# Optimization experiments

Measured on AMD Instinct MI355X. Metric: run time of the kernel, lower is better.

Reference implementation:

```python
import jax, jax.numpy as jnp
import numpy as np

B, S, D = 2, 2048, 1024
H = 16
HD = D // H  # 64

def setup_inputs() -> dict:
    key = jax.random.key(0)
    ks = jax.random.split(key, 6)
    s = 1.0 / np.sqrt(D)
    return {
        "x": jax.random.normal(ks[0], (B, S, D), dtype=jnp.float32),
        "Wq": jax.random.normal(ks[1], (D, D), dtype=jnp.float32) * s,
        "Wk": jax.random.normal(ks[2], (D, D), dtype=jnp.float32) * s,
        "Wv": jax.random.normal(ks[3], (D, D), dtype=jnp.float32) * s,
        "Wo": jax.random.normal(ks[4], (D, D), dtype=jnp.float32) * s,
        "bo": jax.random.normal(ks[5], (D,), dtype=jnp.float32) * 0.01,
    }

def reference(x, Wq, Wk, Wv, Wo, bo):
    b, n, _ = x.shape
    # qkv projections (nn.Linear: x @ W^T, no bias for qkv)
    q = (x @ Wq.T).reshape(b, n, H, HD).transpose(0, 2, 1, 3)  # [B,H,S,hd]
    k = (x @ Wk.T).reshape(b, n, H, HD).transpose(0, 2, 1, 3)
    v = (x @ Wv.T).reshape(b, n, H, HD).transpose(0, 2, 1, 3)
    scores = jnp.einsum('bhqd,bhkd->bhqk', q, k)  # [B,H,S,S]
    causal = jnp.triu(jnp.ones((n, n), dtype=bool), k=1)
    scores = jnp.where(causal, -jnp.inf, scores)
    attn = jax.nn.softmax(scores / np.sqrt(HD), axis=-1)
    ctx = jnp.einsum('bhqk,bhkd->bhqd', attn, v)  # [B,H,S,hd]
    ctx = ctx.transpose(0, 2, 1, 3).reshape(b, n, D)
    return ctx @ Wo.T + bo
```

## Files before the change

kernel.cpp:

```cpp
#include <hip/hip_runtime.h>
#include <hip/hip_bf16.h>

typedef __hip_bfloat16 bf16;
typedef short v8s __attribute__((ext_vector_type(8)));
typedef float v4f __attribute__((ext_vector_type(4)));

#define S_ 2048
#define D_ 1024
#define H_ 16
#define HD_ 64

#define EXP2F(x) __builtin_amdgcn_exp2f(x)
#define NEG_BIG (-1.0e30f)
#define C2 0.1803368801111244f

#define GLDS16(g, l) __builtin_amdgcn_global_load_lds(                        \
    (const __attribute__((address_space(1))) unsigned int*)(g),               \
    (__attribute__((address_space(3))) unsigned int*)(l), 16, 0, 0)

static __device__ __forceinline__ unsigned short bf16_bits(bf16 h) {
    union { bf16 h; unsigned short u; } c; c.h = h; return c.u;
}

static __device__ __forceinline__ v8s pack_bf16x8(const float4 a, const float4 b) {
    union { v8s v; unsigned short u[8]; } r;
    r.u[0] = bf16_bits(__float2bfloat16(a.x));
    r.u[1] = bf16_bits(__float2bfloat16(a.y));
    r.u[2] = bf16_bits(__float2bfloat16(a.z));
    r.u[3] = bf16_bits(__float2bfloat16(a.w));
    r.u[4] = bf16_bits(__float2bfloat16(b.x));
    r.u[5] = bf16_bits(__float2bfloat16(b.y));
    r.u[6] = bf16_bits(__float2bfloat16(b.z));
    r.u[7] = bf16_bits(__float2bfloat16(b.w));
    return r.v;
}

__global__ __launch_bounds__(256)
void cvt_bf16(const float* __restrict__ x,  const float* __restrict__ wq,
              const float* __restrict__ wk, const float* __restrict__ wv,
              const float* __restrict__ wo,
              bf16* __restrict__ xb,  bf16* __restrict__ wqb,
              bf16* __restrict__ wkb, bf16* __restrict__ wvb,
              bf16* __restrict__ wob)
{
    const int seg = blockIdx.y;
    const float* src; bf16* dst; int n;
    switch (seg) {
        case 0: src = x;  dst = xb;  n = 4096 * 1024; break;
        case 1: src = wq; dst = wqb; n = 1024 * 1024; break;
        case 2: src = wk; dst = wkb; n = 1024 * 1024; break;
        case 3: src = wv; dst = wvb; n = 1024 * 1024; break;
        default:src = wo; dst = wob; n = 1024 * 1024; break;
    }
    const int idx = (blockIdx.x * 256 + threadIdx.x) * 8;
    if (idx >= n) return;
    *(v8s*)&dst[idx] = pack_bf16x8(*(const float4*)&src[idx],
                                   *(const float4*)&src[idx + 4]);
}

__global__ __launch_bounds__(256)
void gemm_qkv_f(const bf16* __restrict__ xb, const bf16* __restrict__ wqb,
                const bf16* __restrict__ wkb, const bf16* __restrict__ wvb,
                bf16* __restrict__ qd, bf16* __restrict__ kd, bf16* __restrict__ vtd)
{
    const int mode = blockIdx.z;
    const bf16* __restrict__ W = (mode == 0) ? wqb : (mode == 1) ? wkb : wvb;
    const int m0 = blockIdx.x * 128;
    const int n0 = blockIdx.y * 128;
    __shared__ bf16 As[128 * 32];
    __shared__ bf16 Bs[128 * 32];
    const int t    = threadIdx.x;
    const int lane = t & 63, w = t >> 6;
    const int wr = w >> 1, wc = w & 1;
    const int l15 = lane & 15, quad = lane >> 4;
    const int r16 = lane >> 2, c8 = (lane & 3) * 8;
    v4f acc[4][4] = {};

    const bf16* ga = &xb[(m0 + w*16 + r16) * 1024 + c8];
    const bf16* gb = &W [(n0 + w*16 + r16) * 1024 + c8];
    bf16* la0 = &As[w * 16 * 32];
    bf16* la1 = &As[(64 + w * 16) * 32];
    bf16* lb0 = &Bs[w * 16 * 32];
    bf16* lb1 = &Bs[(64 + w * 16) * 32];

    for (int k0 = 0; k0 < 1024; k0 += 32) {
        __syncthreads();
        GLDS16(ga + k0,             la0);
        GLDS16(ga + k0 + 64 * 1024, la1);
        GLDS16(gb + k0,             lb0);
        GLDS16(gb + k0 + 64 * 1024, lb1);
        __syncthreads();
        v8s a[4], b[4];
#pragma unroll
        for (int mt = 0; mt < 4; mt++) a[mt] = *(const v8s*)&As[(wr*64 + mt*16 + l15)*32 + quad*8];
#pragma unroll
        for (int nt = 0; nt < 4; nt++) b[nt] = *(const v8s*)&Bs[(wc*64 + nt*16 + l15)*32 + quad*8];
#pragma unroll
        for (int mt = 0; mt < 4; mt++)
#pragma unroll
            for (int nt = 0; nt < 4; nt++)
                acc[mt][nt] = __builtin_amdgcn_mfma_f32_16x16x32_bf16(a[mt], b[nt], acc[mt][nt], 0, 0, 0);
    }

    const float qscale = (mode == 0) ? C2 : 1.0f;
#pragma unroll
    for (int mt = 0; mt < 4; mt++) {
        const int mb = m0 + wr*64 + mt*16 + quad*4;
        const int b_ = mb >> 11, s = mb & 2047;
#pragma unroll
        for (int nt = 0; nt < 4; nt++) {
            const int n = n0 + wc*64 + nt*16 + l15;
            const int h = n >> 6, d = n & 63;
            if (mode == 2) {
                unsigned int lo = (unsigned int)bf16_bits(__float2bfloat16(acc[mt][nt][0]))
                                | ((unsigned int)bf16_bits(__float2bfloat16(acc[mt][nt][1])) << 16);
                unsigned int hi = (unsigned int)bf16_bits(__float2bfloat16(acc[mt][nt][2]))
                                | ((unsigned int)bf16_bits(__float2bfloat16(acc[mt][nt][3])) << 16);
                uint2 pv; pv.x = lo; pv.y = hi;
                *(uint2*)&vtd[((b_*H_ + h)*HD_ + d)*S_ + s] = pv;
            } else {
                bf16* __restrict__ dst = (mode == 0) ? qd : kd;
#pragma unroll
                for (int r = 0; r < 4; r++)
                    dst[((b_*H_ + h)*S_ + (s + r))*HD_ + d] = __float2bfloat16(acc[mt][nt][r] * qscale);
            }
        }
    }
}

__global__ __launch_bounds__(256)
void gemm_out_f(const bf16* __restrict__ ctx, const bf16* __restrict__ wob,
                const float* __restrict__ bo, float* __restrict__ out)
{
    const int m0 = blockIdx.x * 128;
    const int n0 = blockIdx.y * 128;
    __shared__ bf16 As[128 * 32];
    __shared__ bf16 Bs[128 * 32];
    const int t    = threadIdx.x;
    const int lane = t & 63, w = t >> 6;
    const int wr = w >> 1, wc = w & 1;
    const int l15 = lane & 15, quad = lane >> 4;
    const int r16 = lane >> 2, c8 = (lane & 3) * 8;
    v4f acc[4][4] = {};

    const bf16* ga = &ctx[(m0 + w*16 + r16) * 1024 + c8];
    const bf16* gb = &wob[(n0 + w*16 + r16) * 1024 + c8];
    bf16* la0 = &As[w * 16 * 32];
    bf16* la1 = &As[(64 + w * 16) * 32];
    bf16* lb0 = &Bs[w * 16 * 32];
    bf16* lb1 = &Bs[(64 + w * 16) * 32];

    for (int k0 = 0; k0 < 1024; k0 += 32) {
        __syncthreads();
        GLDS16(ga + k0,             la0);
        GLDS16(ga + k0 + 64 * 1024, la1);
        GLDS16(gb + k0,             lb0);
        GLDS16(gb + k0 + 64 * 1024, lb1);
        __syncthreads();
        v8s a[4], b[4];
#pragma unroll
        for (int mt = 0; mt < 4; mt++) a[mt] = *(const v8s*)&As[(wr*64 + mt*16 + l15)*32 + quad*8];
#pragma unroll
        for (int nt = 0; nt < 4; nt++) b[nt] = *(const v8s*)&Bs[(wc*64 + nt*16 + l15)*32 + quad*8];
#pragma unroll
        for (int mt = 0; mt < 4; mt++)
#pragma unroll
            for (int nt = 0; nt < 4; nt++)
                acc[mt][nt] = __builtin_amdgcn_mfma_f32_16x16x32_bf16(a[mt], b[nt], acc[mt][nt], 0, 0, 0);
    }

#pragma unroll
    for (int mt = 0; mt < 4; mt++) {
        const int mb = m0 + wr*64 + mt*16 + quad*4;
#pragma unroll
        for (int nt = 0; nt < 4; nt++) {
            const int n = n0 + wc*64 + nt*16 + l15;
            const float bias = bo[n];
#pragma unroll
            for (int r = 0; r < 4; r++)
                out[(mb + r)*1024 + n] = acc[mt][nt][r] + bias;
        }
    }
}

__global__ __launch_bounds__(256)
void gemm_qkv(const float* __restrict__ x, const float* __restrict__ Wq,
              const float* __restrict__ Wk, const float* __restrict__ Wv,
              bf16* __restrict__ qd, bf16* __restrict__ kd, bf16* __restrict__ vtd)
{
    const int mode = blockIdx.z;
    const float* __restrict__ W = (mode == 0) ? Wq : (mode == 1) ? Wk : Wv;
    const int m0 = blockIdx.x * 128;
    const int n0 = blockIdx.y * 128;
    __shared__ bf16 As[128 * 40];
    __shared__ bf16 Bs[128 * 40];
    const int t    = threadIdx.x;
    const int lane = t & 63, w = t >> 6;
    const int wr = w >> 1, wc = w & 1;
    const int l15 = lane & 15, quad = lane >> 4;
    const int srow = t >> 2, scol = (t & 3) * 8;
    v4f acc[4][4] = {};

    for (int k0 = 0; k0 < 1024; k0 += 32) {
        __syncthreads();
        {
            const float* pa = &x[(m0 + srow) * 1024 + k0 + scol];
            *(v8s*)&As[srow*40 + scol] = pack_bf16x8(*(const float4*)pa, *(const float4*)(pa + 4));
            const float* pa2 = pa + 64 * 1024;
            *(v8s*)&As[(srow+64)*40 + scol] = pack_bf16x8(*(const float4*)pa2, *(const float4*)(pa2 + 4));
            const float* pb = &W[(n0 + srow) * 1024 + k0 + scol];
            *(v8s*)&Bs[srow*40 + scol] = pack_bf16x8(*(const float4*)pb, *(const float4*)(pb + 4));
            const float* pb2 = pb + 64 * 1024;
            *(v8s*)&Bs[(srow+64)*40 + scol] = pack_bf16x8(*(const float4*)pb2, *(const float4*)(pb2 + 4));
        }
        __syncthreads();
        v8s a[4], b[4];
#pragma unroll
        for (int mt = 0; mt < 4; mt++) a[mt] = *(const v8s*)&As[(wr*64 + mt*16 + l15)*40 + quad*8];
#pragma unroll
        for (int nt = 0; nt < 4; nt++) b[nt] = *(const v8s*)&Bs[(wc*64 + nt*16 + l15)*40 + quad*8];
#pragma unroll
        for (int mt = 0; mt < 4; mt++)
#pragma unroll
            for (int nt = 0; nt < 4; nt++)
                acc[mt][nt] = __builtin_amdgcn_mfma_f32_16x16x32_bf16(a[mt], b[nt], acc[mt][nt], 0, 0, 0);
    }

    const float qscale = (mode == 0) ? C2 : 1.0f;
#pragma unroll
    for (int mt = 0; mt < 4; mt++) {
        const int mb = m0 + wr*64 + mt*16 + quad*4;
        const int b_ = mb >> 11, s = mb & 2047;
#pragma unroll
        for (int nt = 0; nt < 4; nt++) {
            const int n = n0 + wc*64 + nt*16 + l15;
            const int h = n >> 6, d = n & 63;
            if (mode == 2) {
                unsigned int lo = (unsigned int)bf16_bits(__float2bfloat16(acc[mt][nt][0]))
                                | ((unsigned int)bf16_bits(__float2bfloat16(acc[mt][nt][1])) << 16);
                unsigned int hi = (unsigned int)bf16_bits(__float2bfloat16(acc[mt][nt][2]))
                                | ((unsigned int)bf16_bits(__float2bfloat16(acc[mt][nt][3])) << 16);
                uint2 pv; pv.x = lo; pv.y = hi;
                *(uint2*)&vtd[((b_*H_ + h)*HD_ + d)*S_ + s] = pv;
            } else {
                bf16* __restrict__ dst = (mode == 0) ? qd : kd;
#pragma unroll
                for (int r = 0; r < 4; r++)
                    dst[((b_*H_ + h)*S_ + (s + r))*HD_ + d] = __float2bfloat16(acc[mt][nt][r] * qscale);
            }
        }
    }
}

__global__ __launch_bounds__(256)
void gemm_out(const bf16* __restrict__ ctx, const float* __restrict__ Wo,
              const float* __restrict__ bo, float* __restrict__ out)
{
    const int m0 = blockIdx.x * 128;
    const int n0 = blockIdx.y * 128;
    __shared__ bf16 As[128 * 40];
    __shared__ bf16 Bs[128 * 40];
    const int t    = threadIdx.x;
    const int lane = t & 63, w = t >> 6;
    const int wr = w >> 1, wc = w & 1;
    const int l15 = lane & 15, quad = lane >> 4;
    const int srow = t >> 2, scol = (t & 3) * 8;
    v4f acc[4][4] = {};

    for (int k0 = 0; k0 < 1024; k0 += 32) {
        __syncthreads();
        {
            *(v8s*)&As[srow*40 + scol]      = *(const v8s*)&ctx[(m0+srow)*1024 + k0 + scol];
            *(v8s*)&As[(srow+64)*40 + scol] = *(const v8s*)&ctx[(m0+srow+64)*1024 + k0 + scol];
            const float* pb = &Wo[(n0 + srow) * 1024 + k0 + scol];
            *(v8s*)&Bs[srow*40 + scol] = pack_bf16x8(*(const float4*)pb, *(const float4*)(pb + 4));
            const float* pb2 = pb + 64 * 1024;
            *(v8s*)&Bs[(srow+64)*40 + scol] = pack_bf16x8(*(const float4*)pb2, *(const float4*)(pb2 + 4));
        }
        __syncthreads();
        v8s a[4], b[4];
#pragma unroll
        for (int mt = 0; mt < 4; mt++) a[mt] = *(const v8s*)&As[(wr*64 + mt*16 + l15)*40 + quad*8];
#pragma unroll
        for (int nt = 0; nt < 4; nt++) b[nt] = *(const v8s*)&Bs[(wc*64 + nt*16 + l15)*40 + quad*8];
#pragma unroll
        for (int mt = 0; mt < 4; mt++)
#pragma unroll
            for (int nt = 0; nt < 4; nt++)
                acc[mt][nt] = __builtin_amdgcn_mfma_f32_16x16x32_bf16(a[mt], b[nt], acc[mt][nt], 0, 0, 0);
    }

#pragma unroll
    for (int mt = 0; mt < 4; mt++) {
        const int mb = m0 + wr*64 + mt*16 + quad*4;
#pragma unroll
        for (int nt = 0; nt < 4; nt++) {
            const int n = n0 + wc*64 + nt*16 + l15;
            const float bias = bo[n];
#pragma unroll
            for (int r = 0; r < 4; r++)
                out[(mb + r)*1024 + n] = acc[mt][nt][r] + bias;
        }
    }
}

__global__ __launch_bounds__(256)
void flash_attn(const bf16* __restrict__ qd, const bf16* __restrict__ kd,
                const bf16* __restrict__ vtd, bf16* __restrict__ ctx)
{
    const int qb = 15 - blockIdx.x;
    const int bh = blockIdx.y;
    const int t = threadIdx.x;
    const int lane = t & 63, w = t >> 6;
    const int l15 = lane & 15, quad = lane >> 4;
    const int q0 = qb * 128;

    __shared__ bf16 Ks[2][64 * 72];
    __shared__ bf16 Vs[2][64 * 72];
    __shared__ bf16 Pl[4][16 * 72];

    const int mrow0 = q0 + w * 16;
    const int mrow1 = q0 + 64 + w * 16;

    v8s qf[2][2];
#pragma unroll
    for (int mt = 0; mt < 2; mt++) {
        const bf16* qb_ = qd + (bh*S_ + (mt ? mrow1 : mrow0) + l15) * HD_;
        qf[mt][0] = *(const v8s*)(qb_ + quad*8);
        qf[mt][1] = *(const v8s*)(qb_ + 32 + quad*8);
    }

    v4f o[2][4] = {};
    float ps[2][4] = {};

    const int rowlo = t >> 3, col8 = (t & 7) * 8;
    const int nT = qb * 2 + 2;

    v8s pk0 = *(const v8s*)&kd[(bh*S_ + rowlo)*HD_ + col8];
    v8s pk1 = *(const v8s*)&kd[(bh*S_ + rowlo + 32)*HD_ + col8];
    v8s pv0 = *(const v8s*)&vtd[(bh*HD_ + rowlo)*S_ + col8];
    v8s pv1 = *(const v8s*)&vtd[(bh*HD_ + rowlo + 32)*S_ + col8];

    for (int it = 0; it < nT; ++it) {
        const int c0 = it * 64;
        bf16* Kb = &Ks[it & 1][0];
        bf16* Vb = &Vs[it & 1][0];
        *(v8s*)&Kb[rowlo*72 + col8]      = pk0;
        *(v8s*)&Kb[(rowlo+32)*72 + col8] = pk1;
        *(v8s*)&Vb[rowlo*72 + col8]      = pv0;
        *(v8s*)&Vb[(rowlo+32)*72 + col8] = pv1;
        const int cn = (it + 1 < nT) ? c0 + 64 : 0;
        pk0 = *(const v8s*)&kd[(bh*S_ + cn + rowlo)*HD_ + col8];
        pk1 = *(const v8s*)&kd[(bh*S_ + cn + rowlo + 32)*HD_ + col8];
        pv0 = *(const v8s*)&vtd[(bh*HD_ + rowlo)*S_ + cn + col8];
        pv1 = *(const v8s*)&vtd[(bh*HD_ + rowlo + 32)*S_ + cn + col8];
        __syncthreads();

        if (c0 <= mrow1 + 15) {
            v8s kf[4][2];
#pragma unroll
            for (int kt = 0; kt < 4; kt++) {
                kf[kt][0] = *(const v8s*)&Kb[(kt*16 + l15)*72 + quad*8];
                kf[kt][1] = *(const v8s*)&Kb[(kt*16 + l15)*72 + 32 + quad*8];
            }
            v8s vf[4][2];
#pragma unroll
            for (int dt = 0; dt < 4; dt++) {
                vf[dt][0] = *(const v8s*)&Vs[it & 1][(dt*16 + l15)*72 + quad*8];
                vf[dt][1] = *(const v8s*)&Vs[it & 1][(dt*16 + l15)*72 + 32 + quad*8];
            }

#pragma unroll
            for (int mt = 0; mt < 2; mt++) {
                const int mr = mt ? mrow1 : mrow0;
                if (c0 > mr + 15) continue;
                v4f sc[4] = {};
#pragma unroll
                for (int kt = 0; kt < 4; kt++) {
                    sc[kt] = __builtin_amdgcn_mfma_f32_16x16x32_bf16(qf[mt][0], kf[kt][0], sc[kt], 0, 0, 0);
                    sc[kt] = __builtin_amdgcn_mfma_f32_16x16x32_bf16(qf[mt][1], kf[kt][1], sc[kt], 0, 0, 0);
                }
                const bool full = (c0 + 63 <= mr);
#pragma unroll
                for (int r = 0; r < 4; r++) {
                    const int qg = mr + quad*4 + r;
#pragma unroll
                    for (int kt = 0; kt < 4; kt++) {
                        float s = sc[kt][r];
                        if (!full) {
                            const int kg = c0 + kt*16 + l15;
                            s = (kg <= qg) ? s : NEG_BIG;
                        }
                        const float p = EXP2F(s);
                        sc[kt][r] = p;
                        ps[mt][r] += p;
                    }
                }
                bf16* pw = &Pl[w][0];
#pragma unroll
                for (int kt = 0; kt < 4; kt++)
#pragma unroll
                    for (int r = 0; r < 4; r++)
                        pw[(quad*4 + r)*72 + kt*16 + l15] = __float2bfloat16(sc[kt][r]);
                v8s pf0 = *(const v8s*)&pw[l15*72 + quad*8];
                v8s pf1 = *(const v8s*)&pw[l15*72 + 32 + quad*8];
#pragma unroll
                for (int dt = 0; dt < 4; dt++) {
                    o[mt][dt] = __builtin_amdgcn_mfma_f32_16x16x32_bf16(pf0, vf[dt][0], o[mt][dt], 0, 0, 0);
                    o[mt][dt] = __builtin_amdgcn_mfma_f32_16x16x32_bf16(pf1, vf[dt][1], o[mt][dt], 0, 0, 0);
                }
            }
        }
    }

    const int b_ = bh >> 4, h = bh & 15;
#pragma unroll
    for (int mt = 0; mt < 2; mt++) {
        const int mr = mt ? mrow1 : mrow0;
#pragma unroll
        for (int r = 0; r < 4; r++) {
            float l = ps[mt][r];
#pragma unroll
            for (int off = 1; off < 16; off <<= 1) l += __shfl_xor(l, off);
            const float linv = 1.0f / l;
            const int qg = mr + quad*4 + r;
#pragma unroll
            for (int dt = 0; dt < 4; dt++)
                ctx[(b_*S_ + qg)*D_ + h*HD_ + dt*16 + l15] = __float2bfloat16(o[mt][dt][r] * linv);
        }
    }
}

extern "C" void kernel_launch(void* const* d_in, const int* in_sizes, int n_in,
                              void* d_out, int out_size, void* d_ws, size_t ws_size,
                              hipStream_t stream) {
    const float* x  = (const float*)d_in[0];
    const float* Wq = (const float*)d_in[1];
    const float* Wk = (const float*)d_in[2];
    const float* Wv = (const float*)d_in[3];
    const float* Wo = (const float*)d_in[4];
    const float* bo = (const float*)d_in[5];
    float* out = (float*)d_out;

    const size_t SEG = (size_t)2 * H_ * S_ * HD_;
    bf16* qd  = (bf16*)d_ws;
    bf16* kd  = qd  + SEG;
    bf16* vtd = kd  + SEG;
    bf16* xc  = vtd + SEG;

    const size_t need_fast = (SEG * 4 + 4 * 1024 * 1024) * sizeof(bf16);

    if (ws_size >= need_fast) {
        bf16* wqb = xc + SEG;
        bf16* wkb = wqb + 1024 * 1024;
        bf16* wvb = wkb + 1024 * 1024;
        bf16* wob = wvb + 1024 * 1024;
        cvt_bf16<<<dim3(2048, 5), 256, 0, stream>>>(x, Wq, Wk, Wv, Wo,
                                                    xc, wqb, wkb, wvb, wob);
        gemm_qkv_f<<<dim3(32, 8, 3), 256, 0, stream>>>(xc, wqb, wkb, wvb, qd, kd, vtd);
        flash_attn<<<dim3(16, 32), 256, 0, stream>>>(qd, kd, vtd, xc);
        gemm_out_f<<<dim3(32, 8), 256, 0, stream>>>(xc, wob, bo, out);
    } else {
        gemm_qkv<<<dim3(32, 8, 3), 256, 0, stream>>>(x, Wq, Wk, Wv, qd, kd, vtd);
        flash_attn<<<dim3(16, 32), 256, 0, stream>>>(qd, kd, vtd, xc);
        gemm_out<<<dim3(32, 8), 256, 0, stream>>>(xc, Wo, bo, out);
    }
}
```

Baseline: 223.1 us.

## Split causal attention KV range across two blocks and combine partials

Each query block's KV tiles are split into two equal halves. Each half runs in its own block along grid z, which doubles the number of blocks and evens out the causal work per block. Each half writes unnormalized bf16 partial outputs and per-row exp sums to workspace. A new combine kernel adds the two halves and normalizes. This costs extra global traffic, an extra launch, a larger workspace requirement, and some precision lost by storing partials in bf16.

```diff
diff --git a/kernel.cpp b/kernel.cpp
--- a/kernel.cpp
+++ b/kernel.cpp
@@ -20,6 +20,9 @@
 
 static __device__ __forceinline__ unsigned short bf16_bits(bf16 h) {
     union { bf16 h; unsigned short u; } c; c.h = h; return c.u;
+}
+static __device__ __forceinline__ float bits2f(unsigned short u) {
+    union { float f; unsigned int i; } c; c.i = ((unsigned int)u) << 16; return c.f;
 }
 
 static __device__ __forceinline__ v8s pack_bf16x8(const float4 a, const float4 b) {
@@ -306,15 +309,21 @@
 
 __global__ __launch_bounds__(256)
 void flash_attn(const bf16* __restrict__ qd, const bf16* __restrict__ kd,
-                const bf16* __restrict__ vtd, bf16* __restrict__ ctx)
+                const bf16* __restrict__ vtd, bf16* __restrict__ outp,
+                float* __restrict__ lsum)
 {
     const int qb = 15 - blockIdx.x;
     const int bh = blockIdx.y;
+    const int split = blockIdx.z;
+    const bool dosplit = (gridDim.z == 2);
     const int t = threadIdx.x;
     const int lane = t & 63, w = t >> 6;
     const int l15 = lane & 15, quad = lane >> 4;
     const int q0 = qb * 128;
 
+    const int tbeg = dosplit ? split * (qb + 1) : 0;
+    const int tend = dosplit ? tbeg + qb + 1 : 2 * qb + 2;
+
     __shared__ bf16 Ks[2][64 * 72];
     __shared__ bf16 Vs[2][64 * 72];
     __shared__ bf16 Pl[4][16 * 72];
@@ -334,22 +343,22 @@
     float ps[2][4] = {};
 
     const int rowlo = t >> 3, col8 = (t & 7) * 8;
-    const int nT = qb * 2 + 2;
-
-    v8s pk0 = *(const v8s*)&kd[(bh*S_ + rowlo)*HD_ + col8];
-    v8s pk1 = *(const v8s*)&kd[(bh*S_ + rowlo + 32)*HD_ + col8];
-    v8s pv0 = *(const v8s*)&vtd[(bh*HD_ + rowlo)*S_ + col8];
-    v8s pv1 = *(const v8s*)&vtd[(bh*HD_ + rowlo + 32)*S_ + col8];
-
-    for (int it = 0; it < nT; ++it) {
-        const int c0 = it * 64;
+
+    int c0 = tbeg * 64;
+    v8s pk0 = *(const v8s*)&kd[(bh*S_ + c0 + rowlo)*HD_ + col8];
+    v8s pk1 = *(const v8s*)&kd[(bh*S_ + c0 + rowlo + 32)*HD_ + col8];
+    v8s pv0 = *(const v8s*)&vtd[(bh*HD_ + rowlo)*S_ + c0 + col8];
+    v8s pv1 = *(const v8s*)&vtd[(bh*HD_ + rowlo + 32)*S_ + c0 + col8];
+
+    for (int it = tbeg; it < tend; ++it) {
+        c0 = it * 64;
         bf16* Kb = &Ks[it & 1][0];
         bf16* Vb = &Vs[it & 1][0];
         *(v8s*)&Kb[rowlo*72 + col8]      = pk0;
         *(v8s*)&Kb[(rowlo+32)*72 + col8] = pk1;
         *(v8s*)&Vb[rowlo*72 + col8]      = pv0;
         *(v8s*)&Vb[(rowlo+32)*72 + col8] = pv1;
-        const int cn = (it + 1 < nT) ? c0 + 64 : 0;
+        const int cn = (it + 1 < tend) ? c0 + 64 : tbeg * 64;
         pk0 = *(const v8s*)&kd[(bh*S_ + cn + rowlo)*HD_ + col8];
         pk1 = *(const v8s*)&kd[(bh*S_ + cn + rowlo + 32)*HD_ + col8];
         pv0 = *(const v8s*)&vtd[(bh*HD_ + rowlo)*S_ + cn + col8];
@@ -414,6 +423,8 @@
     }
 
     const int b_ = bh >> 4, h = bh & 15;
+    bf16* __restrict__ po = outp + (size_t)split * (4 * 1024 * 1024);
+    float* __restrict__ ls = lsum + split * (32 * S_);
 #pragma unroll
     for (int mt = 0; mt < 2; mt++) {
         const int mr = mt ? mrow1 : mrow0;
@@ -422,13 +433,39 @@
             float l = ps[mt][r];
 #pragma unroll
             for (int off = 1; off < 16; off <<= 1) l += __shfl_xor(l, off);
-            const float linv = 1.0f / l;
             const int qg = mr + quad*4 + r;
-#pragma unroll
-            for (int dt = 0; dt < 4; dt++)
-                ctx[(b_*S_ + qg)*D_ + h*HD_ + dt*16 + l15] = __float2bfloat16(o[mt][dt][r] * linv);
-        }
-    }
+            if (!dosplit) {
+                const float linv = 1.0f / l;
+#pragma unroll
+                for (int dt = 0; dt < 4; dt++)
+                    outp[(b_*S_ + qg)*D_ + h*HD_ + dt*16 + l15] = __float2bfloat16(o[mt][dt][r] * linv);
+            } else {
+                if (l15 == 0) ls[bh*S_ + qg] = l;
+#pragma unroll
+                for (int dt = 0; dt < 4; dt++)
+                    po[(b_*S_ + qg)*D_ + h*HD_ + dt*16 + l15] = __float2bfloat16(o[mt][dt][r]);
+            }
+        }
+    }
+}
+
+__global__ __launch_bounds__(256)
+void combine_k(const bf16* __restrict__ po, const float* __restrict__ lsum,
+               bf16* __restrict__ ctx)
+{
+    const int idx = (blockIdx.x * 256 + threadIdx.x) * 8;
+    const int row = idx >> 10;
+    const int h = (idx & 1023) >> 6;
+    const int b = row >> 11, s = row & 2047;
+    const int bh = b * 16 + h;
+    const float linv = 1.0f / (lsum[bh*S_ + s] + lsum[32*S_ + bh*S_ + s]);
+    union { v8s v; unsigned short u[8]; } a, c, r;
+    a.v = *(const v8s*)&po[idx];
+    c.v = *(const v8s*)&po[4*1024*1024 + idx];
+#pragma unroll
+    for (int j = 0; j < 8; j++)
+        r.u[j] = bf16_bits(__float2bfloat16((bits2f(a.u[j]) + bits2f(c.u[j])) * linv));
+    *(v8s*)&ctx[idx] = r.v;
 }
 
 extern "C" void kernel_launch(void* const* d_in, const int* in_sizes, int n_in,
@@ -447,22 +484,32 @@
     bf16* kd  = qd  + SEG;
     bf16* vtd = kd  + SEG;
     bf16* xc  = vtd + SEG;
-
-    const size_t need_fast = (SEG * 4 + 4 * 1024 * 1024) * sizeof(bf16);
-
-    if (ws_size >= need_fast) {
-        bf16* wqb = xc + SEG;
-        bf16* wkb = wqb + 1024 * 1024;
-        bf16* wvb = wkb + 1024 * 1024;
-        bf16* wob = wvb + 1024 * 1024;
+    bf16* wqb = xc + SEG;
+    bf16* wkb = wqb + 1024 * 1024;
+    bf16* wvb = wkb + 1024 * 1024;
+    bf16* wob = wvb + 1024 * 1024;
+    bf16* po  = wob + 1024 * 1024;
+    float* lsum = (float*)(po + 2 * SEG);
+
+    const size_t need_fast  = (4 * SEG + 4 * 1024 * 1024) * sizeof(bf16);
+    const size_t need_split = need_fast + 2 * SEG * sizeof(bf16) + 2 * 32 * S_ * sizeof(float);
+
+    if (ws_size >= need_split) {
         cvt_bf16<<<dim3(2048, 5), 256, 0, stream>>>(x, Wq, Wk, Wv, Wo,
                                                     xc, wqb, wkb, wvb, wob);
         gemm_qkv_f<<<dim3(32, 8, 3), 256, 0, stream>>>(xc, wqb, wkb, wvb, qd, kd, vtd);
-        flash_attn<<<dim3(16, 32), 256, 0, stream>>>(qd, kd, vtd, xc);
+        flash_attn<<<dim3(16, 32, 2), 256, 0, stream>>>(qd, kd, vtd, po, lsum);
+        combine_k<<<dim3(2048), 256, 0, stream>>>(po, lsum, xc);
+        gemm_out_f<<<dim3(32, 8), 256, 0, stream>>>(xc, wob, bo, out);
+    } else if (ws_size >= need_fast) {
+        cvt_bf16<<<dim3(2048, 5), 256, 0, stream>>>(x, Wq, Wk, Wv, Wo,
+                                                    xc, wqb, wkb, wvb, wob);
+        gemm_qkv_f<<<dim3(32, 8, 3), 256, 0, stream>>>(xc, wqb, wkb, wvb, qd, kd, vtd);
+        flash_attn<<<dim3(16, 32, 1), 256, 0, stream>>>(qd, kd, vtd, xc, lsum);
         gemm_out_f<<<dim3(32, 8), 256, 0, stream>>>(xc, wob, bo, out);
     } else {
         gemm_qkv<<<dim3(32, 8, 3), 256, 0, stream>>>(x, Wq, Wk, Wv, qd, kd, vtd);
-        flash_attn<<<dim3(16, 32), 256, 0, stream>>>(qd, kd, vtd, xc);
+        flash_attn<<<dim3(16, 32, 1), 256, 0, stream>>>(qd, kd, vtd, xc, (float*)xc);
         gemm_out<<<dim3(32, 8), 256, 0, stream>>>(xc, Wo, bo, out);
     }
 }
```

New measurement: 230.6 us. 1.03x slower.
